# Kernel tuning notes

Hardware: AMD Instinct MI355X
Metric: run time of the kernel (lower is better)

## Reference

```python
import jax, jax.numpy as jnp
import numpy as np

N = 100000
E = 1600000
D = 128
EIG = 32
NUM_MOTIFS = 64
EPS = 1e-8  # torch cosine_similarity eps


def setup_inputs() -> dict:
    key = jax.random.key(0)
    ks = jax.random.split(key, 12)
    return {
        "q": jax.random.normal(ks[0], (N, D), jnp.float32),
        "k": jax.random.normal(ks[1], (N, D), jnp.float32),
        "v": jax.random.normal(ks[2], (N, D), jnp.float32),
        "eigs": jax.random.normal(ks[3], (N, EIG), jnp.float32),
        "motif_adj_vals": jax.random.uniform(ks[4], (E,), jnp.float32),
        "lambda0": jax.random.normal(ks[5], (1,), jnp.float32) * 0.1,
        "gamma": jax.random.normal(ks[6], (1,), jnp.float32) * 0.1,
        "motif_emb_w": jax.random.uniform(ks[7], (NUM_MOTIFS, 1), jnp.float32),
        "row": jax.random.randint(ks[8], (E,), 0, N, jnp.int32),
        "col": jax.random.randint(ks[9], (E,), 0, N, jnp.int32),
        "motif_ids": jax.random.randint(ks[10], (N,), 0, NUM_MOTIFS, jnp.int32),
    }


def _sparse_softmax(vals, row, n):
    # softmax of per-edge values grouped by destination/row index
    m = jax.ops.segment_max(vals, row, num_segments=n)
    e = jnp.exp(vals - m[row])
    z = jax.ops.segment_sum(e, row, num_segments=n)
    return e / z[row]


def reference(q, k, v, eigs, motif_adj_vals, lambda0, gamma, motif_emb_w,
              row, col, motif_ids):
    sqrt_dim = 1.0 / jnp.sqrt(jnp.asarray(q.shape[1], q.dtype))
    # edge-wise q.k dot product, scaled
    x = jnp.sum(q[row] * k[col], axis=-1) * sqrt_dim          # [E]
    # eig branch (args.model contains 'eig'); note original does NOT scale by sqrt_eig
    y = jnp.sum(eigs[row] * eigs[col], axis=-1)               # [E]
    s0 = x + jnp.exp(lambda0[0]) * y
    # motif branch: embedding lookup + cosine similarity along the edge dim (dim=0)
    me = motif_emb_w[motif_ids][:, 0]                          # [N]
    a, b = me[row], me[col]                                    # [E]
    sim = jnp.sum(a * b) / (jnp.maximum(jnp.linalg.norm(a), EPS)
                            * jnp.maximum(jnp.linalg.norm(b), EPS))
    s1 = motif_adj_vals * gamma[0] * sim                       # [E]
    n = q.shape[0]
    attn = 0.5 * (_sparse_softmax(s0, row, n) + _sparse_softmax(s1, row, n))
    # sparse-dense matmul: out[r] = sum_e attn_e * v[col_e]
    return jax.ops.segment_sum(attn[:, None] * v[col], row, num_segments=n)
```

## Files before the change

### kernel.cpp

```cpp
#include <hip/hip_runtime.h>
#include <math.h>

#define N_NODES 100000
#define N_EDGES 1600000
#define DIM 128
#define EIGD 32
#define CS_EPS 1e-8f

#define B1 256
#define CHUNK 6250
#define NB 391

static const size_t OFF_REC    = 0;
static const size_t OFF_SE     = 12800000;
static const size_t OFF_GH     = 25600000;
static const size_t OFF_BSTART = 26000384;
static const size_t OFF_GPART  = 26001952;
static const size_t OFF_OFFS   = 26006048;
static const size_t OFF_SCAL   = 26406064;

__global__ void __launch_bounds__(256) kb_hist(
        const int* __restrict__ row, const int* __restrict__ col,
        const float* __restrict__ motif_w, const int* __restrict__ motif_ids,
        int* __restrict__ gh, float4* __restrict__ gpart) {
    __shared__ int hist[NB];
    __shared__ float wlds[64];
    __shared__ float red[3][4];
    const int t = threadIdx.x, b = blockIdx.x;
    for (int i = t; i < NB; i += 256) hist[i] = 0;
    if (t < 64) wlds[t] = motif_w[t];
    __syncthreads();

    const int e0 = b * CHUNK, e1 = min(N_EDGES, e0 + CHUNK);
    float sab = 0.f, saa = 0.f, sbb = 0.f;
    for (int e = e0 + t; e < e1; e += 256) {
        int r = row[e], c = col[e];
        atomicAdd(&hist[r >> 8], 1);
        float mr = wlds[motif_ids[r]], mc = wlds[motif_ids[c]];
        sab += mr * mc; saa += mr * mr; sbb += mc * mc;
    }
#pragma unroll
    for (int off = 32; off >= 1; off >>= 1) {
        sab += __shfl_xor(sab, off);
        saa += __shfl_xor(saa, off);
        sbb += __shfl_xor(sbb, off);
    }
    int lane = t & 63, wid = t >> 6;
    if (lane == 0) { red[0][wid] = sab; red[1][wid] = saa; red[2][wid] = sbb; }
    __syncthreads();
    if (t == 0) {
        float a = 0.f, bb = 0.f, cc = 0.f;
#pragma unroll
        for (int i = 0; i < 4; i++) { a += red[0][i]; bb += red[1][i]; cc += red[2][i]; }
        gpart[b] = make_float4(a, bb, cc, 0.f);
    }
    __syncthreads();
    for (int i = t; i < NB; i += 256) gh[b * NB + i] = hist[i];
}

__global__ void __launch_bounds__(512) ke_scan(
        int* __restrict__ gh, int* __restrict__ bstart,
        const float4* __restrict__ gpart, const float* __restrict__ gamma,
        float* __restrict__ scal, int* __restrict__ offs) {
    const int t = threadIdx.x;
    __shared__ int tot[512];
    int mytot = 0;
    if (t < NB) {
        int run = 0;
        for (int b = 0; b < B1; b++) {
            int v = gh[b * NB + t];
            gh[b * NB + t] = run;
            run += v;
        }
        mytot = run;
    }
    tot[t] = mytot;
    __syncthreads();
    for (int off = 1; off < 512; off <<= 1) {
        int v = (t >= off) ? tot[t - off] : 0;
        __syncthreads();
        tot[t] += v;
        __syncthreads();
    }
    if (t < NB) bstart[t] = tot[t] - mytot;
    if (t == NB - 1) {
        bstart[NB] = tot[t];
        offs[N_NODES] = tot[t];
    }

    float sab = 0.f, saa = 0.f, sbb = 0.f;
    for (int i = t; i < B1; i += 512) {
        float4 g = gpart[i];
        sab += g.x; saa += g.y; sbb += g.z;
    }
#pragma unroll
    for (int off = 32; off >= 1; off >>= 1) {
        sab += __shfl_xor(sab, off);
        saa += __shfl_xor(saa, off);
        sbb += __shfl_xor(sbb, off);
    }
    __shared__ float red[3][8];
    int lane = t & 63, wid = t >> 6;
    if (lane == 0) { red[0][wid] = sab; red[1][wid] = saa; red[2][wid] = sbb; }
    __syncthreads();
    if (t == 0) {
        float a = 0.f, bb = 0.f, cc = 0.f;
#pragma unroll
        for (int i = 0; i < 8; i++) { a += red[0][i]; bb += red[1][i]; cc += red[2][i]; }
        float na = sqrtf(bb); if (na < CS_EPS) na = CS_EPS;
        float nb2 = sqrtf(cc); if (nb2 < CS_EPS) nb2 = CS_EPS;
        scal[0] = gamma[0] * (a / (na * nb2));
    }
}

__global__ void __launch_bounds__(256) kd_coarse(
        const int* __restrict__ row, const int* __restrict__ col,
        const float* __restrict__ adj, const int* __restrict__ gh,
        const int* __restrict__ bstart, int2* __restrict__ rec) {
    __shared__ int cur[NB];
    const int t = threadIdx.x, b = blockIdx.x;
    for (int i = t; i < NB; i += 256) cur[i] = bstart[i] + gh[b * NB + i];
    __syncthreads();
    const int e0 = b * CHUNK, e1 = min(N_EDGES, e0 + CHUNK);
    for (int e = e0 + t; e < e1; e += 256) {
        int r = row[e];
        int pos = atomicAdd(&cur[r >> 8], 1);
        rec[pos] = make_int2(col[e] | ((r & 255) << 17), __float_as_int(adj[e]));
    }
}

__global__ void __launch_bounds__(256) kf_fine(
        const int2* __restrict__ rec, const int* __restrict__ bstart,
        int* __restrict__ offs, float2* __restrict__ se) {
    __shared__ int hist[256], sc[256], cur[256];
    const int t = threadIdx.x, b = blockIdx.x;
    hist[t] = 0;
    __syncthreads();
    const int s = bstart[b], e1 = bstart[b + 1];
    for (int i = s + t; i < e1; i += 256) {
        int rl = (rec[i].x >> 17) & 255;
        atomicAdd(&hist[rl], 1);
    }
    __syncthreads();
    int v = hist[t];
    sc[t] = v;
    __syncthreads();
    for (int off = 1; off < 256; off <<= 1) {
        int w = (t >= off) ? sc[t - off] : 0;
        __syncthreads();
        sc[t] += w;
        __syncthreads();
    }
    int excl = sc[t] - v;
    int rowg = b * 256 + t;
    if (rowg < N_NODES) offs[rowg] = s + excl;
    cur[t] = s + excl;
    __syncthreads();
    for (int i = s + t; i < e1; i += 256) {
        int2 rc = rec[i];
        int rl = (rc.x >> 17) & 255;
        int pos = atomicAdd(&cur[rl], 1);
        se[pos] = make_float2(__int_as_float(rc.x & 0x1FFFF), __int_as_float(rc.y));
    }
}

__global__ void __launch_bounds__(256) k4_flash(
        const float* __restrict__ q, const float* __restrict__ k,
        const float* __restrict__ eigs, const float* __restrict__ v,
        const float* __restrict__ lambda0, const int* __restrict__ offs,
        const float2* __restrict__ se, const float* __restrict__ scal,
        float* __restrict__ out) {
    const int tid  = threadIdx.x;
    const int lane = tid & 63;
    const int wid  = tid >> 6;
    const int r = blockIdx.x * 4 + wid;
    if (r >= N_NODES) return;
    const int l32  = lane & 31;
    const int half = lane >> 5;
    const float inv_sqrt_d = 0.08838834764831843f;

    const int start = offs[r], end = offs[r + 1];
    if (end == start) {
        ((float2*)(out + (size_t)r * DIM))[lane] = make_float2(0.f, 0.f);
        return;
    }

    const float el0 = expf(lambda0[0]);
    const float cs  = scal[0];

    const float4 qv = ((const float4*)(q + (size_t)r * DIM))[l32];
    const float  er = eigs[(size_t)r * EIGD + l32];

    float m0 = -INFINITY, z0 = 0.f, m1 = -INFINITY, z1 = 0.f;
    float2 acc0 = make_float2(0.f, 0.f), acc1 = make_float2(0.f, 0.f);

    for (int base = start; base < end; base += 2) {
        int e = base + half;
        float s0 = -INFINITY, s1 = -INFINITY;
        int c = 0;
        if (e < end) {
            float2 ea = se[e];
            c = __float_as_int(ea.x);
            const float4 kv = ((const float4*)(k + (size_t)c * DIM))[l32];
            float x = qv.x * kv.x + qv.y * kv.y + qv.z * kv.z + qv.w * kv.w;
            float y = er * eigs[(size_t)c * EIGD + l32];
#pragma unroll
            for (int off = 16; off >= 1; off >>= 1) {
                x += __shfl_xor(x, off);
                y += __shfl_xor(y, off);
            }
            s0 = x * inv_sqrt_d + el0 * y;
            s1 = cs * ea.y;
        }
        float s0a = __shfl(s0, 0),  s0b = __shfl(s0, 32);
        float s1a = __shfl(s1, 0),  s1b = __shfl(s1, 32);
        int   ca  = __shfl(c, 0),   cb  = __shfl(c, 32);
        bool hasB = (base + 1 < end);

        float nm0 = fmaxf(m0, fmaxf(s0a, s0b));
        float r0  = __expf(m0 - nm0);
        float w0a = __expf(s0a - nm0);
        float w0b = hasB ? __expf(s0b - nm0) : 0.f;
        z0 = z0 * r0 + w0a + w0b;
        m0 = nm0;

        float nm1 = fmaxf(m1, fmaxf(s1a, s1b));
        float r1  = __expf(m1 - nm1);
        float w1a = __expf(s1a - nm1);
        float w1b = hasB ? __expf(s1b - nm1) : 0.f;
        z1 = z1 * r1 + w1a + w1b;
        m1 = nm1;

        float2 va = ((const float2*)(v + (size_t)ca * DIM))[lane];
        acc0.x = acc0.x * r0 + w0a * va.x; acc0.y = acc0.y * r0 + w0a * va.y;
        acc1.x = acc1.x * r1 + w1a * va.x; acc1.y = acc1.y * r1 + w1a * va.y;
        if (hasB) {
            float2 vb = ((const float2*)(v + (size_t)cb * DIM))[lane];
            acc0.x += w0b * vb.x; acc0.y += w0b * vb.y;
            acc1.x += w1b * vb.x; acc1.y += w1b * vb.y;
        }
    }

    float iz0 = 1.f / z0, iz1 = 1.f / z1;
    float2 o = make_float2(0.5f * (acc0.x * iz0 + acc1.x * iz1),
                           0.5f * (acc0.y * iz0 + acc1.y * iz1));
    ((float2*)(out + (size_t)r * DIM))[lane] = o;
}

extern "C" void kernel_launch(void* const* d_in, const int* in_sizes, int n_in,
                              void* d_out, int out_size, void* d_ws, size_t ws_size,
                              hipStream_t stream) {
    const float* q        = (const float*)d_in[0];
    const float* k        = (const float*)d_in[1];
    const float* v        = (const float*)d_in[2];
    const float* eigs     = (const float*)d_in[3];
    const float* adj      = (const float*)d_in[4];
    const float* lambda0  = (const float*)d_in[5];
    const float* gamma    = (const float*)d_in[6];
    const float* motif_w  = (const float*)d_in[7];
    const int*   row      = (const int*)d_in[8];
    const int*   col      = (const int*)d_in[9];
    const int*   motif_ids= (const int*)d_in[10];
    float* out = (float*)d_out;

    char* ws = (char*)d_ws;
    int2*   rec    = (int2*)(ws + OFF_REC);
    float2* se     = (float2*)(ws + OFF_SE);
    int*    gh     = (int*)(ws + OFF_GH);
    int*    bstart = (int*)(ws + OFF_BSTART);
    float4* gpart  = (float4*)(ws + OFF_GPART);
    int*    offs   = (int*)(ws + OFF_OFFS);
    float*  scal   = (float*)(ws + OFF_SCAL);

    hipLaunchKernelGGL(kb_hist, dim3(B1), dim3(256), 0, stream,
                       row, col, motif_w, motif_ids, gh, gpart);
    hipLaunchKernelGGL(ke_scan, dim3(1), dim3(512), 0, stream,
                       gh, bstart, gpart, gamma, scal, offs);
    hipLaunchKernelGGL(kd_coarse, dim3(B1), dim3(256), 0, stream,
                       row, col, adj, gh, bstart, rec);
    hipLaunchKernelGGL(kf_fine, dim3(NB), dim3(256), 0, stream,
                       rec, bstart, offs, se);
    hipLaunchKernelGGL(k4_flash, dim3((N_NODES + 3) / 4), dim3(256), 0, stream,
                       q, k, eigs, v, lambda0, offs, se, scal, out);
}
```

Measured before the change: 522.2 us.

## Convert k, v, eigs to bf16 and process four edges per wave

Adds a pre-pass kernel that converts k, v and eigs to bf16 in workspace. The flash aggregation kernel then gathers bf16 rows, which halves the bytes fetched per random neighbour access. It also processes four edges per wave iteration using 16-lane groups, so fewer shuffle steps are needed per edge. The cost is an extra full read and write of k, v and eigs each call, plus reduced precision in the dot products and the V accumulation.

```diff
diff --git a/kernel.cpp b/kernel.cpp
--- a/kernel.cpp
+++ b/kernel.cpp
@@ -18,6 +18,37 @@
 static const size_t OFF_GPART  = 26001952;
 static const size_t OFF_OFFS   = 26006048;
 static const size_t OFF_SCAL   = 26406064;
+static const size_t OFF_KB     = 26406080;
+static const size_t OFF_VB     = 52006080;
+static const size_t OFF_EB     = 77606080;
+
+__device__ __forceinline__ unsigned short f2bf(float f) {
+    unsigned u = __float_as_uint(f);
+    unsigned r = (u + 0x7fffu + ((u >> 16) & 1u)) >> 16;
+    return (unsigned short)r;
+}
+__device__ __forceinline__ float blo(unsigned w) { return __uint_as_float(w << 16); }
+__device__ __forceinline__ float bhi(unsigned w) { return __uint_as_float(w & 0xffff0000u); }
+
+#define K4C 3200000
+#define E4C 800000
+
+__global__ void __launch_bounds__(256) ka_cvt(
+        const float* __restrict__ k, const float* __restrict__ v,
+        const float* __restrict__ eigs,
+        ushort* __restrict__ kb, ushort* __restrict__ vb,
+        ushort* __restrict__ eb) {
+    int i = blockIdx.x * blockDim.x + threadIdx.x;
+    const float* src; ushort* dst; int j;
+    if (i < K4C)            { src = k;    dst = kb; j = i; }
+    else if (i < 2 * K4C)   { src = v;    dst = vb; j = i - K4C; }
+    else if (i < 2*K4C+E4C) { src = eigs; dst = eb; j = i - 2 * K4C; }
+    else return;
+    float4 f = ((const float4*)src)[j];
+    ushort4 o;
+    o.x = f2bf(f.x); o.y = f2bf(f.y); o.z = f2bf(f.z); o.w = f2bf(f.w);
+    ((ushort4*)dst)[j] = o;
+}
 
 __global__ void __launch_bounds__(256) kb_hist(
         const int* __restrict__ row, const int* __restrict__ col,
@@ -165,8 +196,8 @@
 }
 
 __global__ void __launch_bounds__(256) k4_flash(
-        const float* __restrict__ q, const float* __restrict__ k,
-        const float* __restrict__ eigs, const float* __restrict__ v,
+        const float* __restrict__ q, const ushort* __restrict__ kb,
+        const ushort* __restrict__ eb, const ushort* __restrict__ vb,
         const float* __restrict__ lambda0, const int* __restrict__ offs,
         const float2* __restrict__ se, const float* __restrict__ scal,
         float* __restrict__ out) {
@@ -175,8 +206,8 @@
     const int wid  = tid >> 6;
     const int r = blockIdx.x * 4 + wid;
     if (r >= N_NODES) return;
-    const int l32  = lane & 31;
-    const int half = lane >> 5;
+    const int l16 = lane & 15;
+    const int grp = lane >> 4;
     const float inv_sqrt_d = 0.08838834764831843f;
 
     const int start = offs[r], end = offs[r + 1];
@@ -188,56 +219,91 @@
     const float el0 = expf(lambda0[0]);
     const float cs  = scal[0];
 
-    const float4 qv = ((const float4*)(q + (size_t)r * DIM))[l32];
-    const float  er = eigs[(size_t)r * EIGD + l32];
+    const float4* qp = (const float4*)(q + (size_t)r * DIM);
+    const float4 qa = qp[l16 * 2];
+    const float4 qc = qp[l16 * 2 + 1];
+    const unsigned erw = *(const unsigned*)(eb + (size_t)r * EIGD + l16 * 2);
+    const float er0 = blo(erw), er1 = bhi(erw);
 
     float m0 = -INFINITY, z0 = 0.f, m1 = -INFINITY, z1 = 0.f;
     float2 acc0 = make_float2(0.f, 0.f), acc1 = make_float2(0.f, 0.f);
 
-    for (int base = start; base < end; base += 2) {
-        int e = base + half;
-        float s0 = -INFINITY, s1 = -INFINITY;
+    for (int base = start; base < end; base += 4) {
+        int e = base + grp;
+        float s0p = -INFINITY, s1v = -INFINITY;
         int c = 0;
         if (e < end) {
             float2 ea = se[e];
             c = __float_as_int(ea.x);
-            const float4 kv = ((const float4*)(k + (size_t)c * DIM))[l32];
-            float x = qv.x * kv.x + qv.y * kv.y + qv.z * kv.z + qv.w * kv.w;
-            float y = er * eigs[(size_t)c * EIGD + l32];
-#pragma unroll
-            for (int off = 16; off >= 1; off >>= 1) {
-                x += __shfl_xor(x, off);
-                y += __shfl_xor(y, off);
-            }
-            s0 = x * inv_sqrt_d + el0 * y;
-            s1 = cs * ea.y;
-        }
-        float s0a = __shfl(s0, 0),  s0b = __shfl(s0, 32);
-        float s1a = __shfl(s1, 0),  s1b = __shfl(s1, 32);
-        int   ca  = __shfl(c, 0),   cb  = __shfl(c, 32);
-        bool hasB = (base + 1 < end);
-
-        float nm0 = fmaxf(m0, fmaxf(s0a, s0b));
+            s1v = cs * ea.y;
+            const uint4 kw = *(const uint4*)(kb + (size_t)c * DIM + l16 * 8);
+            float x;
+            x = qa.x * blo(kw.x);
+            x = fmaf(qa.y, bhi(kw.x), x);
+            x = fmaf(qa.z, blo(kw.y), x);
+            x = fmaf(qa.w, bhi(kw.y), x);
+            x = fmaf(qc.x, blo(kw.z), x);
+            x = fmaf(qc.y, bhi(kw.z), x);
+            x = fmaf(qc.z, blo(kw.w), x);
+            x = fmaf(qc.w, bhi(kw.w), x);
+            const unsigned ecw = *(const unsigned*)(eb + (size_t)c * EIGD + l16 * 2);
+            float y = er0 * blo(ecw) + er1 * bhi(ecw);
+            s0p = x * inv_sqrt_d + el0 * y;
+        }
+#pragma unroll
+        for (int off = 8; off >= 1; off >>= 1) s0p += __shfl_xor(s0p, off);
+
+        float s00 = __shfl(s0p, 0),  s01 = __shfl(s0p, 16);
+        float s02 = __shfl(s0p, 32), s03 = __shfl(s0p, 48);
+        float s10 = __shfl(s1v, 0),  s11 = __shfl(s1v, 16);
+        float s12 = __shfl(s1v, 32), s13 = __shfl(s1v, 48);
+        int   c0  = __shfl(c, 0),    c1  = __shfl(c, 16);
+        int   c2  = __shfl(c, 32),   c3  = __shfl(c, 48);
+        int cnt = end - base;
+
+        float nm0 = fmaxf(m0, fmaxf(fmaxf(s00, s01), fmaxf(s02, s03)));
         float r0  = __expf(m0 - nm0);
-        float w0a = __expf(s0a - nm0);
-        float w0b = hasB ? __expf(s0b - nm0) : 0.f;
-        z0 = z0 * r0 + w0a + w0b;
+        float w00 = __expf(s00 - nm0);
+        float w01 = __expf(s01 - nm0);
+        float w02 = __expf(s02 - nm0);
+        float w03 = __expf(s03 - nm0);
+        z0 = z0 * r0 + w00 + w01 + w02 + w03;
         m0 = nm0;
 
-        float nm1 = fmaxf(m1, fmaxf(s1a, s1b));
+        float nm1 = fmaxf(m1, fmaxf(fmaxf(s10, s11), fmaxf(s12, s13)));
         float r1  = __expf(m1 - nm1);
-        float w1a = __expf(s1a - nm1);
-        float w1b = hasB ? __expf(s1b - nm1) : 0.f;
-        z1 = z1 * r1 + w1a + w1b;
+        float w10 = __expf(s10 - nm1);
+        float w11 = __expf(s11 - nm1);
+        float w12 = __expf(s12 - nm1);
+        float w13 = __expf(s13 - nm1);
+        z1 = z1 * r1 + w10 + w11 + w12 + w13;
         m1 = nm1;
 
-        float2 va = ((const float2*)(v + (size_t)ca * DIM))[lane];
-        acc0.x = acc0.x * r0 + w0a * va.x; acc0.y = acc0.y * r0 + w0a * va.y;
-        acc1.x = acc1.x * r1 + w1a * va.x; acc1.y = acc1.y * r1 + w1a * va.y;
-        if (hasB) {
-            float2 vb = ((const float2*)(v + (size_t)cb * DIM))[lane];
-            acc0.x += w0b * vb.x; acc0.y += w0b * vb.y;
-            acc1.x += w1b * vb.x; acc1.y += w1b * vb.y;
+        acc0.x *= r0; acc0.y *= r0;
+        acc1.x *= r1; acc1.y *= r1;
+        {
+            unsigned vw = *(const unsigned*)(vb + (size_t)c0 * DIM + lane * 2);
+            float vx = blo(vw), vy = bhi(vw);
+            acc0.x = fmaf(w00, vx, acc0.x); acc0.y = fmaf(w00, vy, acc0.y);
+            acc1.x = fmaf(w10, vx, acc1.x); acc1.y = fmaf(w10, vy, acc1.y);
+        }
+        if (cnt > 1) {
+            unsigned vw = *(const unsigned*)(vb + (size_t)c1 * DIM + lane * 2);
+            float vx = blo(vw), vy = bhi(vw);
+            acc0.x = fmaf(w01, vx, acc0.x); acc0.y = fmaf(w01, vy, acc0.y);
+            acc1.x = fmaf(w11, vx, acc1.x); acc1.y = fmaf(w11, vy, acc1.y);
+        }
+        if (cnt > 2) {
+            unsigned vw = *(const unsigned*)(vb + (size_t)c2 * DIM + lane * 2);
+            float vx = blo(vw), vy = bhi(vw);
+            acc0.x = fmaf(w02, vx, acc0.x); acc0.y = fmaf(w02, vy, acc0.y);
+            acc1.x = fmaf(w12, vx, acc1.x); acc1.y = fmaf(w12, vy, acc1.y);
+        }
+        if (cnt > 3) {
+            unsigned vw = *(const unsigned*)(vb + (size_t)c3 * DIM + lane * 2);
+            float vx = blo(vw), vy = bhi(vw);
+            acc0.x = fmaf(w03, vx, acc0.x); acc0.y = fmaf(w03, vy, acc0.y);
+            acc1.x = fmaf(w13, vx, acc1.x); acc1.y = fmaf(w13, vy, acc1.y);
         }
     }
 
@@ -271,7 +337,12 @@
     float4* gpart  = (float4*)(ws + OFF_GPART);
     int*    offs   = (int*)(ws + OFF_OFFS);
     float*  scal   = (float*)(ws + OFF_SCAL);
-
+    ushort* kb     = (ushort*)(ws + OFF_KB);
+    ushort* vb     = (ushort*)(ws + OFF_VB);
+    ushort* eb     = (ushort*)(ws + OFF_EB);
+
+    hipLaunchKernelGGL(ka_cvt, dim3((2 * K4C + E4C + 255) / 256), dim3(256), 0, stream,
+                       k, v, eigs, kb, vb, eb);
     hipLaunchKernelGGL(kb_hist, dim3(B1), dim3(256), 0, stream,
                        row, col, motif_w, motif_ids, gh, gpart);
     hipLaunchKernelGGL(ke_scan, dim3(1), dim3(512), 0, stream,
@@ -281,5 +352,5 @@
     hipLaunchKernelGGL(kf_fine, dim3(NB), dim3(256), 0, stream,
                        rec, bstart, offs, se);
     hipLaunchKernelGGL(k4_flash, dim3((N_NODES + 3) / 4), dim3(256), 0, stream,
-                       q, k, eigs, v, lambda0, offs, se, scal, out);
-}
+                       q, kb, eb, vb, lambda0, offs, se, scal, out);
+}
```

Result: faster. 477.6 us (-8.5%).
